# Optimization experiments

Hardware: AMD Instinct MI355X
Metric: run time of the kernel (lower is better)

Reference implementation:

```python
import jax, jax.numpy as jnp
import numpy as np

B, S, D, H, DFF, L, V = 2, 512, 768, 12, 3072, 12, 32000
DK = D // H
LN_EPS = 1e-5


def setup_inputs() -> dict:
    key = jax.random.key(0)
    ks = jax.random.split(key, 24)
    s = 0.02
    n = lambda k, shp: (s * jax.random.normal(k, shp)).astype(jnp.float32)
    return dict(
        tokens=jax.random.randint(ks[0], (B, S), 0, V, dtype=jnp.int32),
        tok_emb=n(ks[1], (V, D)),
        pos_emb=n(ks[2], (S, D)),
        ln1_s=jnp.ones((L, D), jnp.float32), ln1_b=jnp.zeros((L, D), jnp.float32),
        Wq=n(ks[3], (L, D, D)), bq=jnp.zeros((L, D), jnp.float32),
        Wk=n(ks[4], (L, D, D)), bk=jnp.zeros((L, D), jnp.float32),
        Wv=n(ks[5], (L, D, D)), bv=jnp.zeros((L, D), jnp.float32),
        Wo=n(ks[6], (L, D, D)), bo=jnp.zeros((L, D), jnp.float32),
        ln2_s=jnp.ones((L, D), jnp.float32), ln2_b=jnp.zeros((L, D), jnp.float32),
        W1=n(ks[7], (L, D, DFF)), b1=jnp.zeros((L, DFF), jnp.float32),
        W2=n(ks[8], (L, DFF, D)), b2=jnp.zeros((L, D), jnp.float32),
        W_out=n(ks[9], (D, V)), b_out=jnp.zeros((V,), jnp.float32),
    )


def _layernorm(x, scale, bias):
    mu = jnp.mean(x, axis=-1, keepdims=True)
    var = jnp.mean(jnp.square(x - mu), axis=-1, keepdims=True)
    return (x - mu) * jax.lax.rsqrt(var + LN_EPS) * scale + bias


def _gpt1_forward(tokens, tok_emb, pos_emb, ln1_s, ln1_b, Wq, bq, Wk, bk, Wv, bv,
                  Wo, bo, ln2_s, ln2_b, W1, b1, W2, b2, W_out, b_out):
    b, s = tokens.shape
    x = tok_emb[tokens] + pos_emb[:s][None]  # [B,S,D]

    def step(x, p):
        (l1s, l1b, wq, bq_, wk, bk_, wv, bv_, wo, bo_, l2s, l2b, w1, b1_, w2, b2_) = p
        x2 = _layernorm(x, l1s, l1b)
        q = (x2 @ wq + bq_).reshape(b, s, H, DK)
        k = (x2 @ wk + bk_).reshape(b, s, H, DK)
        v = (x2 @ wv + bv_).reshape(b, s, H, DK)
        # NOTE: source has no causal mask (full bidirectional attention).
        scores = jnp.einsum('bqhd,bkhd->bhqk', q, k) / jnp.sqrt(jnp.float32(DK))
        attn = jax.nn.softmax(scores, axis=-1)
        ctx = jnp.einsum('bhqk,bkhd->bqhd', attn, v).reshape(b, s, D)
        x = x + ctx @ wo + bo_
        x2 = _layernorm(x, l2s, l2b)
        # torch nn.GELU default = exact (erf) GELU
        h = jax.nn.gelu(x2 @ w1 + b1_, approximate=False)
        x = x + h @ w2 + b2_
        return x, None

    params = (ln1_s, ln1_b, Wq, bq, Wk, bk, Wv, bv, Wo, bo,
              ln2_s, ln2_b, W1, b1, W2, b2)
    x, _ = jax.lax.scan(step, x, params)
    return x @ W_out + b_out  # [B,S,V]


def reference(tokens, tok_emb, pos_emb, ln1_s, ln1_b, Wq, bq, Wk, bk, Wv, bv,
              Wo, bo, ln2_s, ln2_b, W1, b1, W2, b2, W_out, b_out):
    return _gpt1_forward(tokens, tok_emb, pos_emb, ln1_s, ln1_b, Wq, bq, Wk, bk,
                         Wv, bv, Wo, bo, ln2_s, ln2_b, W1, b1, W2, b2, W_out, b_out)
```

## Files before the change

### kernel.cpp

```cpp
#include <hip/hip_runtime.h>
#include <hip/hip_bf16.h>
#include <math.h>

constexpr int BATCH = 2;
constexpr int SEQ   = 512;
constexpr int DM    = 768;
constexpr int NH    = 12;
constexpr int FF    = 3072;
constexpr int NL    = 12;
constexpr int NV    = 32000;
constexpr int HD    = 64;
constexpr int MT    = BATCH * SEQ;
constexpr int QKV   = 3 * DM;

typedef __attribute__((ext_vector_type(8))) short bf16x8;
typedef __attribute__((ext_vector_type(4))) float f32x4;

__device__ __forceinline__ float b2f(ushort u) {
    return __uint_as_float(((unsigned)u) << 16);
}
__device__ __forceinline__ ushort f2b(float f) {
    __hip_bfloat16 h = __float2bfloat16(f);
    return *reinterpret_cast<ushort*>(&h);
}

template<int N>
__device__ __forceinline__ void waitcnt_vm() {
    if constexpr (N == 0) asm volatile("s_waitcnt vmcnt(0)" ::: "memory");
    else if constexpr (N == 2) asm volatile("s_waitcnt vmcnt(2)" ::: "memory");
    else if constexpr (N == 3) asm volatile("s_waitcnt vmcnt(3)" ::: "memory");
    else if constexpr (N == 4) asm volatile("s_waitcnt vmcnt(4)" ::: "memory");
    else if constexpr (N == 6) asm volatile("s_waitcnt vmcnt(6)" ::: "memory");
    else if constexpr (N == 8) asm volatile("s_waitcnt vmcnt(8)" ::: "memory");
}

__global__ void embed_kernel(const int* __restrict__ tokens,
                             const float* __restrict__ tok_emb,
                             const float* __restrict__ pos_emb,
                             float* __restrict__ x) {
    int m = blockIdx.x;
    int s = m % SEQ;
    int t = tokens[m];
    const float* te = tok_emb + (size_t)t * DM;
    const float* pe = pos_emb + (size_t)s * DM;
    float* row = x + (size_t)m * DM;
    for (int d = threadIdx.x; d < DM; d += blockDim.x)
        row[d] = te[d] + pe[d];
}

__global__ __launch_bounds__(256) void wconv_kernel(
        const float* __restrict__ W, ushort* __restrict__ out,
        int K, int N, size_t inLS, size_t outLS, int nOff) {
    int l  = blockIdx.z;
    int n0 = blockIdx.x * 64;
    int k0 = blockIdx.y * 128;
    int tid = threadIdx.x;
    __shared__ float t[2][64][65];
    const float* src = W + (size_t)l * inLS + (size_t)k0 * N + n0;
    int r  = tid >> 4;
    int c4 = (tid & 15) * 4;
#pragma unroll
    for (int i = 0; i < 8; i++) {
        int krow = i * 16 + r;
        float4 v = *(const float4*)(src + (size_t)krow * N + c4);
        float* dstl = &t[krow >> 6][krow & 63][c4];
        dstl[0] = v.x; dstl[1] = v.y; dstl[2] = v.z; dstl[3] = v.w;
    }
    __syncthreads();
    ushort* dst = out + (size_t)l * outLS;
    int kk = (tid & 15) * 8;
    int h  = kk >> 6;
    int kb = kk & 63;
#pragma unroll
    for (int j = 0; j < 4; j++) {
        int n = j * 16 + (tid >> 4);
        ushort o[8];
#pragma unroll
        for (int m = 0; m < 8; m++) o[m] = f2b(t[h][kb + m][n]);
        *(ushort4*)(dst + (size_t)(nOff + n0 + n) * K + k0 + kk)     = *(ushort4*)&o[0];
        *(ushort4*)(dst + (size_t)(nOff + n0 + n) * K + k0 + kk + 4) = *(ushort4*)&o[4];
    }
}

__global__ void biaspack_kernel(const float* __restrict__ bq,
                                const float* __restrict__ bk,
                                const float* __restrict__ bv,
                                float* __restrict__ bqkv) {
    int idx = blockIdx.x * 256 + threadIdx.x;
    if (idx >= NL * QKV) return;
    int l = idx / QKV, c = idx % QKV;
    float v;
    if (c < DM)            v = bq[l * DM + c];
    else if (c < 2 * DM)   v = bk[l * DM + c - DM];
    else                   v = bv[l * DM + c - 2 * DM];
    bqkv[idx] = v;
}

__global__ void cvt_kernel(const float* __restrict__ in, ushort* __restrict__ out, int n) {
    int i = blockIdx.x * 256 + threadIdx.x;
    if (i < n) out[i] = f2b(in[i]);
}

__global__ __launch_bounds__(256) void ln_kernel(const float* __restrict__ x,
                                                 const float* __restrict__ sc,
                                                 const float* __restrict__ bi,
                                                 ushort* __restrict__ y) {
    int m = blockIdx.x;
    int t = threadIdx.x;
    const float* row = x + (size_t)m * DM;
    float vals[3];
    float s0 = 0.f, s1 = 0.f;
#pragma unroll
    for (int i = 0; i < 3; i++) {
        float v = row[t + 256 * i];
        vals[i] = v;
        s0 += v;
        s1 += v * v;
    }
#pragma unroll
    for (int off = 32; off >= 1; off >>= 1) {
        s0 += __shfl_down(s0, off, 64);
        s1 += __shfl_down(s1, off, 64);
    }
    __shared__ float r0[4], r1[4];
    __shared__ float mu_s, rs_s;
    int wid = t >> 6, lane = t & 63;
    if (lane == 0) { r0[wid] = s0; r1[wid] = s1; }
    __syncthreads();
    if (t == 0) {
        float a = r0[0] + r0[1] + r0[2] + r0[3];
        float q = r1[0] + r1[1] + r1[2] + r1[3];
        float mu  = a / DM;
        float var = q / DM - mu * mu;
        mu_s = mu;
        rs_s = rsqrtf(var + 1e-5f);
    }
    __syncthreads();
    float mu = mu_s, rs = rs_s;
    ushort* orow = y + (size_t)m * DM;
#pragma unroll
    for (int i = 0; i < 3; i++) {
        int d = t + 256 * i;
        orow[d] = f2b((vals[i] - mu) * rs * sc[d] + bi[d]);
    }
}

__device__ __forceinline__ void gload_lds16(const void* g, void* l) {
    __builtin_amdgcn_global_load_lds(
        (const __attribute__((address_space(1))) void*)g,
        (__attribute__((address_space(3))) void*)l, 16, 0, 0);
}

template<int BM, int BN, int WM, int WN, int KSTEP, int NBUF, int SPLITK, int ACT,
         bool RES, bool WF32, bool WBF16, bool VT, bool ATOMIC>
__device__ __forceinline__ void gemm_body(
        const ushort* __restrict__ A, const ushort* __restrict__ BT,
        const float* __restrict__ bias, const float* __restrict__ res,
        float* __restrict__ Cf, ushort* __restrict__ Cb, ushort* __restrict__ Vt,
        int M, int N, int K) {
    constexpr int THREADS = WM * WN * 64;
    constexpr int ROWS    = BM + BN;
    constexpr int SEGS    = KSTEP / 8;
    constexpr int SEGSH   = (KSTEP == 32) ? 2 : 3;
    constexpr int RND     = ROWS * KSTEP / (THREADS * 8);
    constexpr int MR      = BM / WM / 16;
    constexpr int NR      = BN / WN / 16;
    constexpr int KCH     = KSTEP / 32;
    constexpr int STRIDE  = ROWS * KSTEP;
    __shared__ ushort S_lds[NBUF * STRIDE];
    int tid = threadIdx.x;
    int il = tid & 63, wv = tid >> 6;

    int p   = blockIdx.x + gridDim.x * blockIdx.y;
    int nwg = gridDim.x * gridDim.y;
    int q8  = nwg >> 3, r8 = nwg & 7;
    int xcd = p & 7, k8 = p >> 3;
    int orig = (xcd < r8 ? xcd * (q8 + 1) : r8 * (q8 + 1) + (xcd - r8) * q8) + k8;
    int bx = orig / gridDim.y;
    int by = orig % gridDim.y;
    int bm = by * BM, bn = bx * BN;

    int kLen  = K / SPLITK;
    int kBase = blockIdx.z * kLen;

    auto swz = [](int row) -> int {
        return (KSTEP == 32) ? ((row >> 1) & 3) : (row & 7);
    };

    const ushort* src[RND];
    int dstOff[RND];
#pragma unroll
    for (int r = 0; r < RND; r++) {
        int f = r * THREADS + tid;
        int row = f >> SEGSH, seg = f & (SEGS - 1);
        int lseg = seg ^ swz(row);
        src[r] = (row < BM ? A + (size_t)(bm + row) * K
                           : BT + (size_t)(bn + row - BM) * K) + kBase + lseg * 8;
        dstOff[r] = (r * THREADS + wv * 64) * 8;
    }

    int wm = wv / WN, wn = wv % WN;
    int lr = il & 15;
    int lg = il >> 4;
    int swzR = swz(lr);
    f32x4 acc[MR][NR] = {};

    int nt = kLen / KSTEP;

#pragma unroll
    for (int b = 0; b < NBUF - 1; b++)
#pragma unroll
        for (int r = 0; r < RND; r++)
            gload_lds16(src[r] + b * KSTEP, &S_lds[b * STRIDE + dstOff[r]]);
    waitcnt_vm<RND * (NBUF - 2)>();
    __builtin_amdgcn_s_barrier();

    int cur = 0;
    for (int t = 0; t < nt; ++t) {
        if (t + NBUF - 1 < nt) {
            int sb = cur + NBUF - 1; if (sb >= NBUF) sb -= NBUF;
            int kofs = (t + NBUF - 1) * KSTEP;
            ushort* Bp = &S_lds[sb * STRIDE];
#pragma unroll
            for (int r = 0; r < RND; r++) gload_lds16(src[r] + kofs, &Bp[dstOff[r]]);
        }

        const ushort* base = &S_lds[cur * STRIDE];
        bf16x8 af[KCH][MR], bfr[KCH][NR];
#pragma unroll
        for (int kk = 0; kk < KCH; kk++) {
            int phys = ((kk * 4 + lg) ^ swzR) * 8;
#pragma unroll
            for (int i = 0; i < MR; i++)
                af[kk][i] = *(const bf16x8*)&base[(wm * (BM / WM) + i * 16 + lr) * KSTEP + phys];
#pragma unroll
            for (int i = 0; i < NR; i++)
                bfr[kk][i] = *(const bf16x8*)&base[(BM + wn * (BN / WN) + i * 16 + lr) * KSTEP + phys];
        }
        __builtin_amdgcn_s_setprio(1);
#pragma unroll
        for (int kk = 0; kk < KCH; kk++)
#pragma unroll
            for (int mi = 0; mi < MR; mi++)
#pragma unroll
                for (int ni = 0; ni < NR; ni++)
                    acc[mi][ni] = __builtin_amdgcn_mfma_f32_16x16x32_bf16(
                        af[kk][mi], bfr[kk][ni], acc[mi][ni], 0, 0, 0);
        __builtin_amdgcn_s_setprio(0);

        if (t + 1 < nt) {
            int k = nt - t - 2;
            if (k > NBUF - 2) k = NBUF - 2;
            switch (k) {
                case 0:  waitcnt_vm<0>(); break;
                case 1:  waitcnt_vm<RND>(); break;
                default: waitcnt_vm<2 * RND>(); break;
            }
            __builtin_amdgcn_s_barrier();
        }
        cur = (cur + 1 == NBUF) ? 0 : cur + 1;
    }

    bool addBias = bias && (SPLITK == 1 || blockIdx.z == 0);
#pragma unroll
    for (int mi = 0; mi < MR; mi++) {
        int row0 = bm + wm * (BM / WM) + mi * 16 + (il >> 4) * 4;
#pragma unroll
        for (int ni = 0; ni < NR; ni++) {
            int col = bn + wn * (BN / WN) + ni * 16 + (il & 15);
            float bv = addBias ? bias[col] : 0.f;
#pragma unroll
            for (int j = 0; j < 4; j++) {
                int r = row0 + j;
                float v = acc[mi][ni][j] + bv;
                if (ACT == 1) v = 0.5f * v * (1.0f + erff(v * 0.70710678118654752f));
                if (RES) v += res[(size_t)r * N + col];
                if (ATOMIC) atomicAdd(&Cf[(size_t)r * N + col], v);
                else if (WF32) Cf[(size_t)r * N + col] = v;
                if (WBF16) {
                    if (VT && bn >= 2 * DM) {
                        int d  = col - 2 * DM;
                        int hh = d >> 6, dd = d & 63;
                        int bb = r >> 9, s = r & (SEQ - 1);
                        Vt[((size_t)(bb * NH + hh) * HD + dd) * SEQ + s] = f2b(v);
                    } else {
                        Cb[(size_t)r * N + col] = f2b(v);
                    }
                }
            }
        }
    }
}

__global__ __launch_bounds__(256) void gemm_qkv(
        const ushort* A, const ushort* BT, const float* bias,
        ushort* Cb, ushort* Vt, int M, int N, int K) {
    gemm_body<64, 64, 2, 2, 64, 3, 1, 0, false, false, true, true, false>(
        A, BT, bias, nullptr, nullptr, Cb, Vt, M, N, K);
}
__global__ __launch_bounds__(256) void gemm_wo(
        const ushort* A, const ushort* BT, const float* bias,
        float* Cf, int M, int N, int K) {
    gemm_body<64, 64, 2, 2, 64, 3, 3, 0, false, false, false, false, true>(
        A, BT, bias, nullptr, Cf, nullptr, nullptr, M, N, K);
}
__global__ __launch_bounds__(256) void gemm_w1(
        const ushort* A, const ushort* BT, const float* bias,
        ushort* Cb, int M, int N, int K) {
    gemm_body<64, 64, 2, 2, 64, 3, 1, 1, false, false, true, false, false>(
        A, BT, bias, nullptr, nullptr, Cb, nullptr, M, N, K);
}
__global__ __launch_bounds__(256) void gemm_w2(
        const ushort* A, const ushort* BT, const float* bias,
        float* Cf, int M, int N, int K) {
    gemm_body<64, 64, 2, 2, 64, 3, 3, 0, false, false, false, false, true>(
        A, BT, bias, nullptr, Cf, nullptr, nullptr, M, N, K);
}
__global__ __launch_bounds__(512) void gemm_logits(
        const ushort* A, const ushort* BT, const float* bias,
        float* Cf, int M, int N, int K) {
    gemm_body<256, 256, 2, 4, 32, 4, 1, 0, false, true, false, false, false>(
        A, BT, bias, nullptr, Cf, nullptr, nullptr, M, N, K);
}

__device__ __forceinline__ char* swzp(void* base, int row, int colByte) {
    return (char*)base + ((row * 128 + colByte) ^ ((row & 7) << 4));
}
__device__ __forceinline__ const char* swzpc(const void* base, int row, int colByte) {
    return (const char*)base + ((row * 128 + colByte) ^ ((row & 7) << 4));
}

__global__ __launch_bounds__(256) void fattn_kernel(
        const ushort* __restrict__ qkv, const ushort* __restrict__ vt,
        ushort* __restrict__ ctx) {
    int qt = blockIdx.x;
    int h  = blockIdx.y;
    int b  = blockIdx.z;
    int tid = threadIdx.x;
    int il = tid & 63, wv = tid >> 6;
    int qsub = wv & 1, grp = wv >> 1;

    __shared__ __align__(16) char smem[41 * 1024];
    ushort* Ks = (ushort*)(smem + grp * 8192);
    ushort* Vs = (ushort*)(smem + 16384 + grp * 8192);
    ushort* Ps = (ushort*)(smem + 32768 + wv * 2048);
    float*  Om = (float*)smem;
    float*  Ss = (float*)(smem + 16384);

    int bh = b * NH + h;
    const ushort* kbase = qkv + (size_t)b * SEQ * QKV + DM + h * HD;
    const ushort* vbase = vt + (size_t)bh * HD * SEQ;

    int lr = il & 15, lg = il >> 4;
    int qrow = qt * 32 + qsub * 16 + lr;
    const ushort* qptr = qkv + (size_t)(b * SEQ + qrow) * QKV + h * HD + lg * 8;
    bf16x8 qf0 = *(const bf16x8*)qptr;
    bf16x8 qf1 = *(const bf16x8*)(qptr + 32);

    f32x4 accO[4] = {};
    float sm[4] = {0.f, 0.f, 0.f, 0.f};

    int lig  = qsub * 64 + il;
    int srow = lig >> 3;
    int sseg = (lig & 7) * 8;

    bf16x8 kreg[4], vreg[4];
    {
        int k0 = grp * 256;
#pragma unroll
        for (int r = 0; r < 4; r++) {
            int row = r * 16 + srow;
            kreg[r] = *(const bf16x8*)(kbase + (size_t)(k0 + row) * QKV + sseg);
            vreg[r] = *(const bf16x8*)(vbase + (size_t)row * SEQ + k0 + sseg);
        }
    }

    for (int kt = 0; kt < 4; kt++) {
        __syncthreads();
#pragma unroll
        for (int r = 0; r < 4; r++) {
            int row = r * 16 + srow;
            *(bf16x8*)swzp(Ks, row, sseg * 2) = kreg[r];
            *(bf16x8*)swzp(Vs, row, sseg * 2) = vreg[r];
        }
        __syncthreads();

        if (kt < 3) {
            int k0n = grp * 256 + (kt + 1) * 64;
#pragma unroll
            for (int r = 0; r < 4; r++) {
                int row = r * 16 + srow;
                kreg[r] = *(const bf16x8*)(kbase + (size_t)(k0n + row) * QKV + sseg);
                vreg[r] = *(const bf16x8*)(vbase + (size_t)row * SEQ + k0n + sseg);
            }
        }

        f32x4 accS[4] = {};
        __builtin_amdgcn_s_setprio(1);
#pragma unroll
        for (int nf = 0; nf < 4; nf++) {
            bf16x8 b0 = *(const bf16x8*)swzpc(Ks, nf * 16 + lr, lg * 16);
            bf16x8 b1 = *(const bf16x8*)swzpc(Ks, nf * 16 + lr, 64 + lg * 16);
            accS[nf] = __builtin_amdgcn_mfma_f32_16x16x32_bf16(qf0, b0, accS[nf], 0, 0, 0);
            accS[nf] = __builtin_amdgcn_mfma_f32_16x16x32_bf16(qf1, b1, accS[nf], 0, 0, 0);
        }
        __builtin_amdgcn_s_setprio(0);

        float pv[4][4];
#pragma unroll
        for (int nf = 0; nf < 4; nf++)
#pragma unroll
            for (int j = 0; j < 4; j++)
                pv[nf][j] = __expf(fmaf(accS[nf][j], 0.125f, -8.0f));
#pragma unroll
        for (int j = 0; j < 4; j++) {
            float rs = (pv[0][j] + pv[1][j]) + (pv[2][j] + pv[3][j]);
            rs += __shfl_xor(rs, 1, 64);
            rs += __shfl_xor(rs, 2, 64);
            rs += __shfl_xor(rs, 4, 64);
            rs += __shfl_xor(rs, 8, 64);
            sm[j] += rs;
        }

#pragma unroll
        for (int nf = 0; nf < 4; nf++)
#pragma unroll
            for (int j = 0; j < 4; j++)
                *(ushort*)swzp(Ps, lg * 4 + j, (nf * 16 + lr) * 2) = f2b(pv[nf][j]);

        bf16x8 pa0 = *(const bf16x8*)swzpc(Ps, lr, lg * 16);
        bf16x8 pa1 = *(const bf16x8*)swzpc(Ps, lr, 64 + lg * 16);
        __builtin_amdgcn_s_setprio(1);
#pragma unroll
        for (int nf = 0; nf < 4; nf++) {
            bf16x8 v0 = *(const bf16x8*)swzpc(Vs, nf * 16 + lr, lg * 16);
            bf16x8 v1 = *(const bf16x8*)swzpc(Vs, nf * 16 + lr, 64 + lg * 16);
            accO[nf] = __builtin_amdgcn_mfma_f32_16x16x32_bf16(pa0, v0, accO[nf], 0, 0, 0);
            accO[nf] = __builtin_amdgcn_mfma_f32_16x16x32_bf16(pa1, v1, accO[nf], 0, 0, 0);
        }
        __builtin_amdgcn_s_setprio(0);
    }

    __syncthreads();
    if (grp == 1) {
#pragma unroll
        for (int nf = 0; nf < 4; nf++)
#pragma unroll
            for (int j = 0; j < 4; j++)
                Om[(qsub * 16 + lg * 4 + j) * 64 + nf * 16 + lr] = accO[nf][j];
        if (lr == 0) {
#pragma unroll
            for (int j = 0; j < 4; j++)
                Ss[qsub * 16 + lg * 4 + j] = sm[j];
        }
    }
    __syncthreads();
    if (grp == 0) {
        ushort* obase = ctx + (size_t)(b * SEQ + qt * 32 + qsub * 16) * DM + h * HD;
#pragma unroll
        for (int j = 0; j < 4; j++) {
            int q = lg * 4 + j;
            float inv = 1.0f / (sm[j] + Ss[qsub * 16 + q]);
#pragma unroll
            for (int nf = 0; nf < 4; nf++) {
                int d = nf * 16 + lr;
                float o1 = Om[(qsub * 16 + q) * 64 + d];
                obase[(size_t)q * DM + d] = f2b((accO[nf][j] + o1) * inv);
            }
        }
    }
}

extern "C" void kernel_launch(void* const* d_in, const int* in_sizes, int n_in,
                              void* d_out, int out_size, void* d_ws, size_t ws_size,
                              hipStream_t stream) {
    const int*   tokens  = (const int*)d_in[0];
    const float* tok_emb = (const float*)d_in[1];
    const float* pos_emb = (const float*)d_in[2];
    const float* ln1_s   = (const float*)d_in[3];
    const float* ln1_b   = (const float*)d_in[4];
    const float* Wq      = (const float*)d_in[5];
    const float* bq      = (const float*)d_in[6];
    const float* Wk      = (const float*)d_in[7];
    const float* bk      = (const float*)d_in[8];
    const float* Wv      = (const float*)d_in[9];
    const float* bv      = (const float*)d_in[10];
    const float* Wo      = (const float*)d_in[11];
    const float* bo      = (const float*)d_in[12];
    const float* ln2_s   = (const float*)d_in[13];
    const float* ln2_b   = (const float*)d_in[14];
    const float* W1      = (const float*)d_in[15];
    const float* b1      = (const float*)d_in[16];
    const float* W2      = (const float*)d_in[17];
    const float* b2      = (const float*)d_in[18];
    const float* W_out   = (const float*)d_in[19];
    const float* b_out   = (const float*)d_in[20];

    char* ws = (char*)d_ws;
    size_t off = 0;
    auto alloc = [&](size_t bytes) { size_t o = off; off = (off + bytes + 255) & ~(size_t)255; return o; };

    float*  x    = (float*)(ws + alloc((size_t)MT * DM * 4));
    ushort* x2b  = (ushort*)(ws + alloc((size_t)MT * DM * 2));
    ushort* qkvb = (ushort*)(ws + alloc((size_t)MT * QKV * 2));
    ushort* cb   = (ushort*)(ws + alloc((size_t)MT * DM * 2));
    ushort* hb   = (ushort*)(ws + alloc((size_t)MT * FF * 2));
    ushort* xb   = (ushort*)(ws + alloc((size_t)MT * DM * 2));
    ushort* vtb  = (ushort*)(ws + alloc((size_t)BATCH * NH * HD * SEQ * 2));
    float*  bqkv = (float*)(ws + alloc((size_t)NL * QKV * 4));

    size_t szQkvT = (size_t)NL * QKV * DM;
    size_t szWoT  = (size_t)NL * DM * DM;
    size_t szW1T  = (size_t)NL * FF * DM;
    size_t szW2T  = (size_t)NL * DM * FF;
    size_t szWoutT= (size_t)NV * DM;

    size_t actEnd = off;
    size_t fullNeed = actEnd + 2 * (szQkvT + szWoT + szW1T + szW2T + szWoutT) + 5 * 256;
    bool full = (fullNeed <= ws_size);

    ushort *WqkvT, *WoT, *W1T, *W2T, *WoutT;
    if (full) {
        WqkvT = (ushort*)(ws + alloc(szQkvT * 2));
        WoT   = (ushort*)(ws + alloc(szWoT * 2));
        W1T   = (ushort*)(ws + alloc(szW1T * 2));
        W2T   = (ushort*)(ws + alloc(szW2T * 2));
        WoutT = (ushort*)(ws + alloc(szWoutT * 2));
    } else {
        size_t layerElems = (size_t)QKV * DM + (size_t)DM * DM + 2 * (size_t)FF * DM;
        size_t regionElems = layerElems > szWoutT ? layerElems : szWoutT;
        ushort* region = (ushort*)(ws + alloc(regionElems * 2));
        WqkvT = region;
        WoT   = WqkvT + (size_t)QKV * DM;
        W1T   = WoT + (size_t)DM * DM;
        W2T   = W1T + (size_t)FF * DM;
        WoutT = region;
    }

    biaspack_kernel<<<(NL * QKV + 255) / 256, 256, 0, stream>>>(bq, bk, bv, bqkv);
    embed_kernel<<<MT, 256, 0, stream>>>(tokens, tok_emb, pos_emb, x);

    if (full) {
        dim3 gD(DM / 64, DM / 128, NL);
        wconv_kernel<<<gD, 256, 0, stream>>>(Wq, WqkvT, DM, DM, (size_t)DM * DM, (size_t)QKV * DM, 0);
        wconv_kernel<<<gD, 256, 0, stream>>>(Wk, WqkvT, DM, DM, (size_t)DM * DM, (size_t)QKV * DM, DM);
        wconv_kernel<<<gD, 256, 0, stream>>>(Wv, WqkvT, DM, DM, (size_t)DM * DM, (size_t)QKV * DM, 2 * DM);
        wconv_kernel<<<gD, 256, 0, stream>>>(Wo, WoT, DM, DM, (size_t)DM * DM, (size_t)DM * DM, 0);
        dim3 g1(FF / 64, DM / 128, NL);
        wconv_kernel<<<g1, 256, 0, stream>>>(W1, W1T, DM, FF, (size_t)DM * FF, (size_t)FF * DM, 0);
        dim3 g2(DM / 64, FF / 128, NL);
        wconv_kernel<<<g2, 256, 0, stream>>>(W2, W2T, FF, DM, (size_t)FF * DM, (size_t)DM * FF, 0);
        dim3 go(NV / 64, DM / 128, 1);
        wconv_kernel<<<go, 256, 0, stream>>>(W_out, WoutT, DM, NV, 0, 0, 0);
    }

    for (int l = 0; l < NL; l++) {
        ushort* wqkv = WqkvT + (full ? (size_t)l * QKV * DM : 0);
        ushort* wo   = WoT   + (full ? (size_t)l * DM * DM  : 0);
        ushort* w1   = W1T   + (full ? (size_t)l * FF * DM  : 0);
        ushort* w2   = W2T   + (full ? (size_t)l * DM * FF  : 0);
        if (!full) {
            dim3 gD(DM / 64, DM / 128, 1);
            wconv_kernel<<<gD, 256, 0, stream>>>(Wq + (size_t)l * DM * DM, wqkv, DM, DM, 0, 0, 0);
            wconv_kernel<<<gD, 256, 0, stream>>>(Wk + (size_t)l * DM * DM, wqkv, DM, DM, 0, 0, DM);
            wconv_kernel<<<gD, 256, 0, stream>>>(Wv + (size_t)l * DM * DM, wqkv, DM, DM, 0, 0, 2 * DM);
            wconv_kernel<<<gD, 256, 0, stream>>>(Wo + (size_t)l * DM * DM, wo, DM, DM, 0, 0, 0);
            dim3 g1(FF / 64, DM / 128, 1);
            wconv_kernel<<<g1, 256, 0, stream>>>(W1 + (size_t)l * DM * FF, w1, DM, FF, 0, 0, 0);
            dim3 g2(DM / 64, FF / 128, 1);
            wconv_kernel<<<g2, 256, 0, stream>>>(W2 + (size_t)l * FF * DM, w2, FF, DM, 0, 0, 0);
        }

        ln_kernel<<<MT, 256, 0, stream>>>(x, ln1_s + l * DM, ln1_b + l * DM, x2b);

        gemm_qkv<<<dim3(QKV / 64, MT / 64), 256, 0, stream>>>(
            x2b, wqkv, bqkv + (size_t)l * QKV, qkvb, vtb, MT, QKV, DM);

        fattn_kernel<<<dim3(SEQ / 32, NH, BATCH), 256, 0, stream>>>(qkvb, vtb, cb);

        gemm_wo<<<dim3(DM / 64, MT / 64, 3), 256, 0, stream>>>(
            cb, wo, bo + (size_t)l * DM, x, MT, DM, DM);

        ln_kernel<<<MT, 256, 0, stream>>>(x, ln2_s + l * DM, ln2_b + l * DM, x2b);

        gemm_w1<<<dim3(FF / 64, MT / 64), 256, 0, stream>>>(
            x2b, w1, b1 + (size_t)l * FF, hb, MT, FF, DM);

        gemm_w2<<<dim3(DM / 64, MT / 64, 3), 256, 0, stream>>>(
            hb, w2, b2 + (size_t)l * DM, x, MT, DM, FF);
    }

    if (!full) {
        dim3 go(NV / 64, DM / 128, 1);
        wconv_kernel<<<go, 256, 0, stream>>>(W_out, WoutT, DM, NV, 0, 0, 0);
    }
    cvt_kernel<<<(MT * DM + 255) / 256, 256, 0, stream>>>(x, xb, MT * DM);

    gemm_logits<<<dim3(NV / 256, MT / 256), 512, 0, stream>>>(
        xb, WoutT, b_out, (float*)d_out, MT, NV, DM);
}
```

Measured before the change: 1.162 ms.

## Split attention keys across four waves per 16-query tile; shrink logits GEMM tile

The attention kernel now gives each block 16 queries instead of 32. Each of the four waves handles its own 128-key slice with private K/V shared-memory buffers and no per-tile barriers, and the partial outputs and softmax sums are combined through shared memory at the end. This doubles the grid size and removes the register-prefetch double buffering, so more blocks can hide latency, at the cost of 72KB of LDS per block. Separately, the logits GEMM drops to 128x256 tiles with 3 pipeline stages and a min-occupancy launch bound, doubling its block count.

```diff
diff --git a/kernel.cpp b/kernel.cpp
--- a/kernel.cpp
+++ b/kernel.cpp
@@ -32,6 +32,8 @@
     else if constexpr (N == 4) asm volatile("s_waitcnt vmcnt(4)" ::: "memory");
     else if constexpr (N == 6) asm volatile("s_waitcnt vmcnt(6)" ::: "memory");
     else if constexpr (N == 8) asm volatile("s_waitcnt vmcnt(8)" ::: "memory");
+    else if constexpr (N == 12) asm volatile("s_waitcnt vmcnt(12)" ::: "memory");
+    else if constexpr (N == 16) asm volatile("s_waitcnt vmcnt(16)" ::: "memory");
 }
 
 __global__ void embed_kernel(const int* __restrict__ tokens,
@@ -316,10 +318,10 @@
     gemm_body<64, 64, 2, 2, 64, 3, 3, 0, false, false, false, false, true>(
         A, BT, bias, nullptr, Cf, nullptr, nullptr, M, N, K);
 }
-__global__ __launch_bounds__(512) void gemm_logits(
+__global__ __launch_bounds__(512, 4) void gemm_logits(
         const ushort* A, const ushort* BT, const float* bias,
         float* Cf, int M, int N, int K) {
-    gemm_body<256, 256, 2, 4, 32, 4, 1, 0, false, true, false, false, false>(
+    gemm_body<128, 256, 2, 4, 32, 3, 1, 0, false, true, false, false, false>(
         A, BT, bias, nullptr, Cf, nullptr, nullptr, M, N, K);
 }
 
@@ -338,12 +340,11 @@
     int b  = blockIdx.z;
     int tid = threadIdx.x;
     int il = tid & 63, wv = tid >> 6;
-    int qsub = wv & 1, grp = wv >> 1;
-
-    __shared__ __align__(16) char smem[41 * 1024];
-    ushort* Ks = (ushort*)(smem + grp * 8192);
-    ushort* Vs = (ushort*)(smem + 16384 + grp * 8192);
-    ushort* Ps = (ushort*)(smem + 32768 + wv * 2048);
+
+    __shared__ __align__(16) char smem[72 * 1024];
+    ushort* Ks = (ushort*)(smem + wv * 16384);
+    ushort* Vs = (ushort*)(smem + wv * 16384 + 8192);
+    ushort* Ps = (ushort*)(smem + 65536 + wv * 2048);
     float*  Om = (float*)smem;
     float*  Ss = (float*)(smem + 16384);
 
@@ -352,7 +353,7 @@
     const ushort* vbase = vt + (size_t)bh * HD * SEQ;
 
     int lr = il & 15, lg = il >> 4;
-    int qrow = qt * 32 + qsub * 16 + lr;
+    int qrow = qt * 16 + lr;
     const ushort* qptr = qkv + (size_t)(b * SEQ + qrow) * QKV + h * HD + lg * 8;
     bf16x8 qf0 = *(const bf16x8*)qptr;
     bf16x8 qf1 = *(const bf16x8*)(qptr + 32);
@@ -360,39 +361,18 @@
     f32x4 accO[4] = {};
     float sm[4] = {0.f, 0.f, 0.f, 0.f};
 
-    int lig  = qsub * 64 + il;
-    int srow = lig >> 3;
-    int sseg = (lig & 7) * 8;
-
-    bf16x8 kreg[4], vreg[4];
-    {
-        int k0 = grp * 256;
-#pragma unroll
-        for (int r = 0; r < 4; r++) {
-            int row = r * 16 + srow;
-            kreg[r] = *(const bf16x8*)(kbase + (size_t)(k0 + row) * QKV + sseg);
-            vreg[r] = *(const bf16x8*)(vbase + (size_t)row * SEQ + k0 + sseg);
-        }
-    }
-
-    for (int kt = 0; kt < 4; kt++) {
-        __syncthreads();
-#pragma unroll
-        for (int r = 0; r < 4; r++) {
-            int row = r * 16 + srow;
-            *(bf16x8*)swzp(Ks, row, sseg * 2) = kreg[r];
-            *(bf16x8*)swzp(Vs, row, sseg * 2) = vreg[r];
-        }
-        __syncthreads();
-
-        if (kt < 3) {
-            int k0n = grp * 256 + (kt + 1) * 64;
-#pragma unroll
-            for (int r = 0; r < 4; r++) {
-                int row = r * 16 + srow;
-                kreg[r] = *(const bf16x8*)(kbase + (size_t)(k0n + row) * QKV + sseg);
-                vreg[r] = *(const bf16x8*)(vbase + (size_t)row * SEQ + k0n + sseg);
-            }
+    int srow = il >> 3;
+    int sseg = (il & 7) * 8;
+
+    for (int kt = 0; kt < 2; kt++) {
+        int k0 = wv * 128 + kt * 64;
+#pragma unroll
+        for (int r = 0; r < 8; r++) {
+            int row = r * 8 + srow;
+            bf16x8 kv = *(const bf16x8*)(kbase + (size_t)(k0 + row) * QKV + sseg);
+            bf16x8 vv = *(const bf16x8*)(vbase + (size_t)row * SEQ + k0 + sseg);
+            *(bf16x8*)swzp(Ks, row, sseg * 2) = kv;
+            *(bf16x8*)swzp(Vs, row, sseg * 2) = vv;
         }
 
         f32x4 accS[4] = {};
@@ -442,32 +422,25 @@
     }
 
     __syncthreads();
-    if (grp == 1) {
-#pragma unroll
-        for (int nf = 0; nf < 4; nf++)
-#pragma unroll
-            for (int j = 0; j < 4; j++)
-                Om[(qsub * 16 + lg * 4 + j) * 64 + nf * 16 + lr] = accO[nf][j];
-        if (lr == 0) {
-#pragma unroll
-            for (int j = 0; j < 4; j++)
-                Ss[qsub * 16 + lg * 4 + j] = sm[j];
-        }
+#pragma unroll
+    for (int nf = 0; nf < 4; nf++)
+#pragma unroll
+        for (int j = 0; j < 4; j++)
+            Om[((size_t)wv * 16 + lg * 4 + j) * 64 + nf * 16 + lr] = accO[nf][j];
+    if (lr == 0) {
+#pragma unroll
+        for (int j = 0; j < 4; j++)
+            Ss[wv * 16 + lg * 4 + j] = sm[j];
     }
     __syncthreads();
-    if (grp == 0) {
-        ushort* obase = ctx + (size_t)(b * SEQ + qt * 32 + qsub * 16) * DM + h * HD;
-#pragma unroll
-        for (int j = 0; j < 4; j++) {
-            int q = lg * 4 + j;
-            float inv = 1.0f / (sm[j] + Ss[qsub * 16 + q]);
-#pragma unroll
-            for (int nf = 0; nf < 4; nf++) {
-                int d = nf * 16 + lr;
-                float o1 = Om[(qsub * 16 + q) * 64 + d];
-                obase[(size_t)q * DM + d] = f2b((accO[nf][j] + o1) * inv);
-            }
-        }
+    ushort* obase = ctx + (size_t)(b * SEQ + qt * 16) * DM + h * HD;
+#pragma unroll
+    for (int i = 0; i < 4; i++) {
+        int e = i * 256 + tid;
+        int q = e >> 6, d = e & 63;
+        float o = Om[e] + Om[1024 + e] + Om[2048 + e] + Om[3072 + e];
+        float s = Ss[q] + Ss[16 + q] + Ss[32 + q] + Ss[48 + q];
+        obase[(size_t)q * DM + d] = f2b(o / s);
     }
 }
 
@@ -576,7 +549,7 @@
         gemm_qkv<<<dim3(QKV / 64, MT / 64), 256, 0, stream>>>(
             x2b, wqkv, bqkv + (size_t)l * QKV, qkvb, vtb, MT, QKV, DM);
 
-        fattn_kernel<<<dim3(SEQ / 32, NH, BATCH), 256, 0, stream>>>(qkvb, vtb, cb);
+        fattn_kernel<<<dim3(SEQ / 16, NH, BATCH), 256, 0, stream>>>(qkvb, vtb, cb);
 
         gemm_wo<<<dim3(DM / 64, MT / 64, 3), 256, 0, stream>>>(
             cb, wo, bo + (size_t)l * DM, x, MT, DM, DM);
@@ -596,6 +569,6 @@
     }
     cvt_kernel<<<(MT * DM + 255) / 256, 256, 0, stream>>>(x, xb, MT * DM);
 
-    gemm_logits<<<dim3(NV / 256, MT / 256), 512, 0, stream>>>(
+    gemm_logits<<<dim3(NV / 256, MT / 128), 512, 0, stream>>>(
         xb, WoutT, b_out, (float*)d_out, MT, NV, DM);
 }
```

After: 1.182 ms. No clear change (+1.7%).

## Replace split-K atomics with partial buffers reduced inside LayerNorm

Applied to the files above, without the earlier changes.

The split-K Wo and W2 GEMMs now write each K-slice's result to a separate partial buffer with plain stores instead of atomicAdd into the residual stream. The following LayerNorm kernel (and a final fold kernel before the logits GEMM) sums the residual and the three partials, writes the updated residual back, and normalizes. This removes atomic contention and makes the sum order deterministic, at the cost of extra memory traffic for three fp32 partial tensors per residual update.

```diff
diff --git a/kernel.cpp b/kernel.cpp
--- a/kernel.cpp
+++ b/kernel.cpp
@@ -96,15 +96,18 @@
     bqkv[idx] = v;
 }
 
-__global__ void cvt_kernel(const float* __restrict__ in, ushort* __restrict__ out, int n) {
+__global__ void fold_kernel(const float* __restrict__ x, const float* __restrict__ pb,
+                            ushort* __restrict__ out, int n) {
     int i = blockIdx.x * 256 + threadIdx.x;
-    if (i < n) out[i] = f2b(in[i]);
+    if (i < n) out[i] = f2b(x[i] + pb[i] + pb[n + i] + pb[2 * n + i]);
 }
 
 __global__ __launch_bounds__(256) void ln_kernel(const float* __restrict__ x,
+                                                 const float* __restrict__ pb,
                                                  const float* __restrict__ sc,
                                                  const float* __restrict__ bi,
-                                                 ushort* __restrict__ y) {
+                                                 ushort* __restrict__ y,
+                                                 float* __restrict__ xw) {
     int m = blockIdx.x;
     int t = threadIdx.x;
     const float* row = x + (size_t)m * DM;
@@ -112,10 +115,20 @@
     float s0 = 0.f, s1 = 0.f;
 #pragma unroll
     for (int i = 0; i < 3; i++) {
-        float v = row[t + 256 * i];
+        int d = t + 256 * i;
+        float v = row[d];
+        if (pb) {
+            size_t idx = (size_t)m * DM + d;
+            v += pb[idx] + pb[(size_t)MT * DM + idx] + pb[2 * (size_t)MT * DM + idx];
+        }
         vals[i] = v;
         s0 += v;
         s1 += v * v;
+    }
+    if (pb) {
+        float* wrow = xw + (size_t)m * DM;
+#pragma unroll
+        for (int i = 0; i < 3; i++) wrow[t + 256 * i] = vals[i];
     }
 #pragma unroll
     for (int off = 32; off >= 1; off >>= 1) {
@@ -152,7 +165,7 @@
 }
 
 template<int BM, int BN, int WM, int WN, int KSTEP, int NBUF, int SPLITK, int ACT,
-         bool RES, bool WF32, bool WBF16, bool VT, bool ATOMIC>
+         bool RES, bool WF32, bool WBF16, bool VT, bool PART>
 __device__ __forceinline__ void gemm_body(
         const ushort* __restrict__ A, const ushort* __restrict__ BT,
         const float* __restrict__ bias, const float* __restrict__ res,
@@ -262,6 +275,7 @@
     }
 
     bool addBias = bias && (SPLITK == 1 || blockIdx.z == 0);
+    size_t partOfs = PART ? (size_t)blockIdx.z * M * N : 0;
 #pragma unroll
     for (int mi = 0; mi < MR; mi++) {
         int row0 = bm + wm * (BM / WM) + mi * 16 + (il >> 4) * 4;
@@ -275,7 +289,7 @@
                 float v = acc[mi][ni][j] + bv;
                 if (ACT == 1) v = 0.5f * v * (1.0f + erff(v * 0.70710678118654752f));
                 if (RES) v += res[(size_t)r * N + col];
-                if (ATOMIC) atomicAdd(&Cf[(size_t)r * N + col], v);
+                if (PART) Cf[partOfs + (size_t)r * N + col] = v;
                 else if (WF32) Cf[(size_t)r * N + col] = v;
                 if (WBF16) {
                     if (VT && bn >= 2 * DM) {
@@ -300,9 +314,9 @@
 }
 __global__ __launch_bounds__(256) void gemm_wo(
         const ushort* A, const ushort* BT, const float* bias,
-        float* Cf, int M, int N, int K) {
+        float* Pf, int M, int N, int K) {
     gemm_body<64, 64, 2, 2, 64, 3, 3, 0, false, false, false, false, true>(
-        A, BT, bias, nullptr, Cf, nullptr, nullptr, M, N, K);
+        A, BT, bias, nullptr, Pf, nullptr, nullptr, M, N, K);
 }
 __global__ __launch_bounds__(256) void gemm_w1(
         const ushort* A, const ushort* BT, const float* bias,
@@ -312,9 +326,9 @@
 }
 __global__ __launch_bounds__(256) void gemm_w2(
         const ushort* A, const ushort* BT, const float* bias,
-        float* Cf, int M, int N, int K) {
+        float* Pf, int M, int N, int K) {
     gemm_body<64, 64, 2, 2, 64, 3, 3, 0, false, false, false, false, true>(
-        A, BT, bias, nullptr, Cf, nullptr, nullptr, M, N, K);
+        A, BT, bias, nullptr, Pf, nullptr, nullptr, M, N, K);
 }
 __global__ __launch_bounds__(512) void gemm_logits(
         const ushort* A, const ushort* BT, const float* bias,
@@ -501,6 +515,7 @@
     auto alloc = [&](size_t bytes) { size_t o = off; off = (off + bytes + 255) & ~(size_t)255; return o; };
 
     float*  x    = (float*)(ws + alloc((size_t)MT * DM * 4));
+    float*  pbuf = (float*)(ws + alloc(3 * (size_t)MT * DM * 4));
     ushort* x2b  = (ushort*)(ws + alloc((size_t)MT * DM * 2));
     ushort* qkvb = (ushort*)(ws + alloc((size_t)MT * QKV * 2));
     ushort* cb   = (ushort*)(ws + alloc((size_t)MT * DM * 2));
@@ -571,7 +586,8 @@
             wconv_kernel<<<g2, 256, 0, stream>>>(W2 + (size_t)l * FF * DM, w2, FF, DM, 0, 0, 0);
         }
 
-        ln_kernel<<<MT, 256, 0, stream>>>(x, ln1_s + l * DM, ln1_b + l * DM, x2b);
+        ln_kernel<<<MT, 256, 0, stream>>>(x, l == 0 ? nullptr : pbuf,
+                                          ln1_s + l * DM, ln1_b + l * DM, x2b, x);
 
         gemm_qkv<<<dim3(QKV / 64, MT / 64), 256, 0, stream>>>(
             x2b, wqkv, bqkv + (size_t)l * QKV, qkvb, vtb, MT, QKV, DM);
@@ -579,22 +595,23 @@
         fattn_kernel<<<dim3(SEQ / 32, NH, BATCH), 256, 0, stream>>>(qkvb, vtb, cb);
 
         gemm_wo<<<dim3(DM / 64, MT / 64, 3), 256, 0, stream>>>(
-            cb, wo, bo + (size_t)l * DM, x, MT, DM, DM);
-
-        ln_kernel<<<MT, 256, 0, stream>>>(x, ln2_s + l * DM, ln2_b + l * DM, x2b);
+            cb, wo, bo + (size_t)l * DM, pbuf, MT, DM, DM);
+
+        ln_kernel<<<MT, 256, 0, stream>>>(x, pbuf,
+                                          ln2_s + l * DM, ln2_b + l * DM, x2b, x);
 
         gemm_w1<<<dim3(FF / 64, MT / 64), 256, 0, stream>>>(
             x2b, w1, b1 + (size_t)l * FF, hb, MT, FF, DM);
 
         gemm_w2<<<dim3(DM / 64, MT / 64, 3), 256, 0, stream>>>(
-            hb, w2, b2 + (size_t)l * DM, x, MT, DM, FF);
+            hb, w2, b2 + (size_t)l * DM, pbuf, MT, DM, FF);
     }
 
     if (!full) {
         dim3 go(NV / 64, DM / 128, 1);
         wconv_kernel<<<go, 256, 0, stream>>>(W_out, WoutT, DM, NV, 0, 0, 0);
     }
-    cvt_kernel<<<(MT * DM + 255) / 256, 256, 0, stream>>>(x, xb, MT * DM);
+    fold_kernel<<<(MT * DM + 255) / 256, 256, 0, stream>>>(x, pbuf, xb, MT * DM);
 
     gemm_logits<<<dim3(NV / 256, MT / 256), 512, 0, stream>>>(
         xb, WoutT, b_out, (float*)d_out, MT, NV, DM);
```

After: 1.116 ms. 1.04x faster.
